# Optimization experiments

Measured on AMD Instinct MI355X. Metric: run time of the kernel, lower is better.

Reference implementation:

```python
import jax, jax.numpy as jnp
import numpy as np

DIM = 128; MOTION = 128; HEADS = 8; WS = 8; B2 = 4; H = 192; W = 192; HID = 512

def _ln(x, w, b, eps=1e-5):
    m = x.mean(-1, keepdims=True)
    v = ((x - m) ** 2).mean(-1, keepdims=True)
    return (x - m) / jnp.sqrt(v + eps) * w + b

def _win_part(x, ws):
    B, Hh, Ww, C = x.shape
    x = x.reshape(B, Hh // ws, ws, Ww // ws, ws, C).transpose(0, 1, 3, 2, 4, 5)
    return x.reshape(-1, ws * ws, C)

def _win_rev(win, ws, Hh, Ww):
    nwB, N, C = win.shape
    B = nwB // ((Hh // ws) * (Ww // ws))
    x = win.reshape(B, Hh // ws, Ww // ws, ws, ws, C).transpose(0, 1, 3, 2, 4, 5)
    return x.reshape(B, Hh, Ww, C)

def setup_inputs() -> dict:
    key = jax.random.key(0)
    ks = jax.random.split(key, 12)
    def lin(k, o, i):
        return jax.random.normal(k, (o, i), jnp.float32) * 0.02
    return {
        "x": jax.random.normal(ks[0], (B2, H * W, DIM), jnp.float32),
        "cor": jax.random.uniform(ks[1], (B2, H * W, 2), dtype=jnp.float32),
        "q_w": lin(ks[2], DIM, DIM),
        "kv_w": lin(ks[3], 2 * DIM, DIM),
        "cor_w": lin(ks[4], MOTION, 2),
        "proj_w": lin(ks[5], DIM, DIM), "proj_b": jnp.zeros((DIM,), jnp.float32),
        "mproj_w": lin(ks[6], MOTION, MOTION), "mproj_b": jnp.zeros((MOTION,), jnp.float32),
        "norm1_w": jnp.ones((DIM,), jnp.float32), "norm1_b": jnp.zeros((DIM,), jnp.float32),
        "norm2_w": jnp.ones((DIM,), jnp.float32), "norm2_b": jnp.zeros((DIM,), jnp.float32),
        "fc1_w": lin(ks[7], HID, DIM), "fc1_b": jnp.zeros((HID,), jnp.float32),
        "dw_w": jax.random.normal(ks[8], (HID, 1, 3, 3), jnp.float32) * 0.1,
        "dw_b": jnp.zeros((HID,), jnp.float32),
        "fc2_w": lin(ks[9], DIM, HID), "fc2_b": jnp.zeros((DIM,), jnp.float32),
    }

def _attn(x1, x2, cor, q_w, kv_w, cor_w, proj_w, proj_b, mproj_w, mproj_b):
    # x1,x2: (nwB, N, C) windowed query / cross-frame key-value; cor: (nwB, N, 2)
    B, N, C = x1.shape
    hd = C // HEADS
    mh = MOTION // HEADS
    scale = hd ** -0.5
    q = (x1 @ q_w.T).reshape(B, N, HEADS, hd).transpose(0, 2, 1, 3)
    kv = (x2 @ kv_w.T).reshape(B, N, 2, HEADS, hd).transpose(2, 0, 3, 1, 4)
    k, v = kv[0], kv[1]
    ce = cor @ cor_w.T                                   # (B, N, MOTION)
    ceh = ce.reshape(B, N, HEADS, mh).transpose(0, 2, 1, 3)
    attn = jax.nn.softmax(jnp.einsum('bhnd,bhmd->bhnm', q, k) * scale, axis=-1)
    xo = jnp.einsum('bhnm,bhmd->bhnd', attn, v).transpose(0, 2, 1, 3).reshape(B, N, C)
    crev = jnp.einsum('bhnm,bhmd->bhnd', attn, ceh).transpose(0, 2, 1, 3).reshape(B, N, MOTION)
    motion = (crev - ce) @ mproj_w.T + mproj_b
    return xo @ proj_w.T + proj_b, motion

def _mlp(x, fc1_w, fc1_b, dw_w, dw_b, fc2_w, fc2_b):
    B, N, _ = x.shape
    h = x @ fc1_w.T + fc1_b                              # (B, N, HID)
    hm = h.transpose(0, 2, 1).reshape(B, HID, H, W)
    hm = jax.lax.conv_general_dilated(hm, dw_w, (1, 1), 'SAME',
                                      feature_group_count=HID,
                                      dimension_numbers=('NCHW', 'OIHW', 'NCHW'))
    hm = hm + dw_b[None, :, None, None]
    h = jax.nn.gelu(hm.reshape(B, HID, N).transpose(0, 2, 1), approximate=False)
    return h @ fc2_w.T + fc2_b

def reference(x, cor, q_w, kv_w, cor_w, proj_w, proj_b, mproj_w, mproj_b,
              norm1_w, norm1_b, norm2_w, norm2_b, fc1_w, fc1_b, dw_w, dw_b, fc2_w, fc2_b):
    shortcut = x
    xn = _ln(x, norm1_w, norm1_b).reshape(B2, H, W, DIM)
    cm = cor.reshape(B2, H, W, 2)
    xw = _win_part(xn, WS)                               # (nwB, 64, DIM)
    cw = _win_part(cm, WS)
    nwB = xw.shape[0]
    xr = jnp.concatenate([xw[nwB // 2:], xw[:nwB // 2]], axis=0)
    xa, xm = _attn(xw, xr, cw, q_w, kv_w, cor_w, proj_w, proj_b, mproj_w, mproj_b)
    xa = _win_rev(xa, WS, H, W).reshape(B2, H * W, DIM)
    xm = _win_rev(xm, WS, H, W).reshape(B2, H * W, MOTION)
    x = shortcut + xa
    x = x + _mlp(_ln(x, norm2_w, norm2_b), fc1_w, fc1_b, dw_w, dw_b, fc2_w, fc2_b)
    return x, xm
```

## Files before the change

kernel.cpp:

```cpp
#include <hip/hip_runtime.h>
#include <hip/hip_bf16.h>
#include <math.h>

#define NB 4
#define IMG 192
#define HW (IMG*IMG)
#define T_TOT (NB*HW)
#define HID 512
#define NWB 2304
#define WPB 576
#define NWS 24

typedef __bf16 bf16;
typedef __bf16 bf8 __attribute__((ext_vector_type(8)));
typedef __bf16 bf4 __attribute__((ext_vector_type(4)));
typedef float f32x4 __attribute__((ext_vector_type(4)));

#define MFMA(a,b,c) __builtin_amdgcn_mfma_f32_16x16x32_bf16(a,b,c,0,0,0)

#define BAR_LGKM asm volatile("s_waitcnt lgkmcnt(0)\ns_barrier" ::: "memory")
#define BAR_ALL  asm volatile("s_waitcnt vmcnt(0) lgkmcnt(0)\ns_barrier" ::: "memory")

__device__ __forceinline__ int swz128(int row, int col){ return row*128 + (col ^ ((row&7)<<3)); }

__device__ __forceinline__ bf8 zero_bf8(){
  bf8 z = { (bf16)0.f,(bf16)0.f,(bf16)0.f,(bf16)0.f,(bf16)0.f,(bf16)0.f,(bf16)0.f,(bf16)0.f };
  return z;
}
__device__ __forceinline__ f32x4 zero_f4(){ f32x4 z = {0.f,0.f,0.f,0.f}; return z; }

typedef const __attribute__((address_space(1))) unsigned int as1_u32;
typedef __attribute__((address_space(3))) unsigned int as3_u32;
__device__ __forceinline__ void gload16(const bf16* g, bf16* l){
  __builtin_amdgcn_global_load_lds((as1_u32*)g, (as3_u32*)l, 16, 0, 0);
}

__global__ __launch_bounds__(256) void k_prep(
    const float* __restrict__ q_w, const float* __restrict__ kv_w,
    const float* __restrict__ proj_w, const float* __restrict__ fc1w,
    const float* __restrict__ fc2w, const float* __restrict__ mproj_w,
    const float* __restrict__ cor_w,
    bf16* __restrict__ wq, bf16* __restrict__ wkv, bf16* __restrict__ wpj,
    bf16* __restrict__ wf1, bf16* __restrict__ wf2, bf16* __restrict__ a2w)
{
  int idx = blockIdx.x*256 + threadIdx.x;
  if (idx < 16384){ wq[idx] = (bf16)(q_w[idx]*0.25f); return; }
  idx -= 16384;
  if (idx < 32768){ wkv[idx] = (bf16)kv_w[idx]; return; }
  idx -= 32768;
  if (idx < 16384){ wpj[idx] = (bf16)proj_w[idx]; return; }
  idx -= 16384;
  if (idx < 65536){ wf1[idx] = (bf16)fc1w[idx]; return; }
  idx -= 65536;
  if (idx < 65536){ wf2[idx] = (bf16)fc2w[idx]; return; }
  idx -= 65536;
  if (idx >= 4096) return;
  int o = idx >> 5, k = idx & 31;
  float acc = 0.f;
  if (k < 16){
    int h = k >> 1, c = k & 1;
    #pragma unroll
    for (int i=0;i<16;i++)
      acc += mproj_w[o*128 + h*16 + i] * cor_w[(h*16+i)*2 + c];
  }
  a2w[o*32 + k] = (bf16)acc;
}

__global__ __launch_bounds__(256) void k_attn(
    const float* __restrict__ x_in, const float* __restrict__ cor,
    const float* __restrict__ n1w, const float* __restrict__ n1b,
    const bf16* __restrict__ wq, const bf16* __restrict__ wkv,
    const bf16* __restrict__ wpj, const bf16* __restrict__ a2w,
    const float* __restrict__ proj_b, const float* __restrict__ mproj_b,
    bf16* __restrict__ x1, float* __restrict__ out_m)
{
  __shared__ __align__(16) bf16 s_s [64*128];
  __shared__ __align__(16) bf16 s_k [64*128];
  __shared__ __align__(16) bf16 s_vT[128*64];
  __shared__ __align__(16) bf16 s_P [64*64];
  __shared__ __align__(16) bf16 s_cT[16*64];
  __shared__ __align__(16) bf16 s_D [64*32];

  int tid = threadIdx.x, wm = tid>>6, l = tid&63;
  int lr = l & 15, lg = l >> 4;
  int win = blockIdx.x;
  int b  = win / WPB, wi = win % WPB;
  int wy = wi / NWS,  wx = wi % NWS;
  int bp = (b + NB/2) % NB;

  float cwf = 0.f;
  if (tid < 128){
    int m = tid >> 1, c = tid & 1;
    cwf = cor[((size_t)b*HW + (size_t)(wy*8+(m>>3))*IMG + wx*8+(m&7))*2 + c];
  }

  *(unsigned long long*)&s_D[tid*8]   = 0ull;
  *(unsigned long long*)&s_D[tid*8+4] = 0ull;
  if (tid >= 192){
    int cc = tid - 192;
    #pragma unroll
    for (int r=3;r<16;r++) s_cT[r*64 + cc] = (bf16)0.f;
  }
  if (tid < 128){
    int c = tid & 1, m = tid >> 1;
    s_cT[c*64 + (m ^ (c<<3))] = (bf16)cwf;
  } else if (tid < 192){
    int m = tid - 128;
    s_cT[2*64 + (m ^ 16)] = (bf16)1.0f;
  }

  {
    float4 nw0 = *(const float4*)(n1w + lr*8), nw1 = *(const float4*)(n1w + lr*8 + 4);
    float4 nb0 = *(const float4*)(n1b + lr*8), nb1 = *(const float4*)(n1b + lr*8 + 4);
    #pragma unroll
    for (int p=0;p<4;p++){
      int n = wm*16 + p*4 + lg;
      const float* xp = x_in + ((size_t)bp*HW + (size_t)(wy*8+(n>>3))*IMG + wx*8+(n&7))*128 + lr*8;
      float4 a = *(const float4*)xp;
      float4 b4 = *(const float4*)(xp+4);
      float s  = a.x+a.y+a.z+a.w + b4.x+b4.y+b4.z+b4.w;
      float sq = a.x*a.x+a.y*a.y+a.z*a.z+a.w*a.w + b4.x*b4.x+b4.y*b4.y+b4.z*b4.z+b4.w*b4.w;
      #pragma unroll
      for (int m=1;m<16;m<<=1){ s += __shfl_xor(s,m,16); sq += __shfl_xor(sq,m,16); }
      float mean = s*(1.f/128.f), var = sq*(1.f/128.f) - mean*mean;
      float rstd = rsqrtf(var + 1e-5f);
      bf8 o;
      o[0] = (bf16)((a.x -mean)*rstd*nw0.x + nb0.x);
      o[1] = (bf16)((a.y -mean)*rstd*nw0.y + nb0.y);
      o[2] = (bf16)((a.z -mean)*rstd*nw0.z + nb0.z);
      o[3] = (bf16)((a.w -mean)*rstd*nw0.w + nb0.w);
      o[4] = (bf16)((b4.x-mean)*rstd*nw1.x + nb1.x);
      o[5] = (bf16)((b4.y-mean)*rstd*nw1.y + nb1.y);
      o[6] = (bf16)((b4.z-mean)*rstd*nw1.z + nb1.z);
      o[7] = (bf16)((b4.w-mean)*rstd*nw1.w + nb1.w);
      *(bf8*)&s_s[swz128(n, lr*8)] = o;
    }
  }

  {
    bf8 af[4];
    #pragma unroll
    for (int ks=0;ks<4;ks++) af[ks] = *(const bf8*)&s_s[swz128(wm*16+lr, ks*32 + lg*8)];
    #pragma unroll
    for (int nt=0;nt<8;nt++){
      f32x4 acc = zero_f4();
      #pragma unroll
      for (int ks=0;ks<4;ks++){
        bf8 bfr = *(const bf8*)(wkv + (nt*16+lr)*128 + ks*32 + lg*8);
        acc = MFMA(af[ks], bfr, acc);
      }
      #pragma unroll
      for (int j=0;j<4;j++){
        int row = wm*16 + lg*4 + j;
        s_k[swz128(row, nt*16+lr)] = (bf16)acc[j];
      }
    }
    #pragma unroll
    for (int nt=0;nt<8;nt++){
      f32x4 acc = zero_f4();
      #pragma unroll
      for (int ks=0;ks<4;ks++){
        bf8 bfr = *(const bf8*)(wkv + (128 + nt*16+lr)*128 + ks*32 + lg*8);
        acc = MFMA(af[ks], bfr, acc);
      }
      #pragma unroll
      for (int j=0;j<4;j++){
        int tok = wm*16 + lg*4 + j;
        int chc = nt*16 + lr;
        s_vT[chc*64 + (tok ^ ((chc&7)<<3))] = (bf16)acc[j];
      }
    }
  }

  {
    float4 nw0 = *(const float4*)(n1w + lr*8), nw1 = *(const float4*)(n1w + lr*8 + 4);
    float4 nb0 = *(const float4*)(n1b + lr*8), nb1 = *(const float4*)(n1b + lr*8 + 4);
    #pragma unroll
    for (int p=0;p<4;p++){
      int n = wm*16 + p*4 + lg;
      const float* xp = x_in + ((size_t)b*HW + (size_t)(wy*8+(n>>3))*IMG + wx*8+(n&7))*128 + lr*8;
      float4 a = *(const float4*)xp;
      float4 b4 = *(const float4*)(xp+4);
      float s  = a.x+a.y+a.z+a.w + b4.x+b4.y+b4.z+b4.w;
      float sq = a.x*a.x+a.y*a.y+a.z*a.z+a.w*a.w + b4.x*b4.x+b4.y*b4.y+b4.z*b4.z+b4.w*b4.w;
      #pragma unroll
      for (int m=1;m<16;m<<=1){ s += __shfl_xor(s,m,16); sq += __shfl_xor(sq,m,16); }
      float mean = s*(1.f/128.f), var = sq*(1.f/128.f) - mean*mean;
      float rstd = rsqrtf(var + 1e-5f);
      bf8 o;
      o[0] = (bf16)((a.x -mean)*rstd*nw0.x + nb0.x);
      o[1] = (bf16)((a.y -mean)*rstd*nw0.y + nb0.y);
      o[2] = (bf16)((a.z -mean)*rstd*nw0.z + nb0.z);
      o[3] = (bf16)((a.w -mean)*rstd*nw0.w + nb0.w);
      o[4] = (bf16)((b4.x-mean)*rstd*nw1.x + nb1.x);
      o[5] = (bf16)((b4.y-mean)*rstd*nw1.y + nb1.y);
      o[6] = (bf16)((b4.z-mean)*rstd*nw1.z + nb1.z);
      o[7] = (bf16)((b4.w-mean)*rstd*nw1.w + nb1.w);
      *(bf8*)&s_s[swz128(n, lr*8)] = o;
    }
  }

  {
    bf8 af[4];
    #pragma unroll
    for (int ks=0;ks<4;ks++) af[ks] = *(const bf8*)&s_s[swz128(wm*16+lr, ks*32 + lg*8)];
    #pragma unroll
    for (int nt=0;nt<8;nt++){
      f32x4 acc = zero_f4();
      #pragma unroll
      for (int ks=0;ks<4;ks++){
        bf8 bfr = *(const bf8*)(wq + (nt*16+lr)*128 + ks*32 + lg*8);
        acc = MFMA(af[ks], bfr, acc);
      }
      #pragma unroll
      for (int j=0;j<4;j++){
        int row = wm*16 + lg*4 + j;
        s_s[swz128(row, nt*16+lr)] = (bf16)acc[j];
      }
    }
  }

  BAR_LGKM;

  float mycw[4] = {0.f,0.f,0.f,0.f};
  if (lr < 2){
    #pragma unroll
    for (int j=0;j<4;j++){
      int row = wm*16 + lg*4 + j;
      mycw[j] = (float)s_cT[lr*64 + (row ^ (lr<<3))];
    }
  }

  f32x4 accS[4];
  {
    bf8 aS = zero_bf8();
    if (l < 32) aS = *(const bf8*)&s_s[swz128(wm*16+lr, lg*8)];
    #pragma unroll
    for (int nt=0;nt<4;nt++){
      bf8 bSv = zero_bf8();
      if (l < 32) bSv = *(const bf8*)&s_k[swz128(nt*16+lr, lg*8)];
      accS[nt] = MFMA(aS, bSv, zero_f4());
    }
  }
  #pragma unroll
  for (int h=0;h<8;h++){
    #pragma unroll
    for (int nt=0;nt<4;nt++){
      #pragma unroll
      for (int j=0;j<4;j++){
        int row = wm*16 + lg*4 + j;
        s_P[row*64 + ((nt*16+lr) ^ ((row&7)<<3))] = (bf16)__expf(accS[nt][j]);
      }
    }
    if (h < 7){
      bf8 aS = zero_bf8();
      if (l < 32) aS = *(const bf8*)&s_s[swz128(wm*16+lr, (h+1)*16 + lg*8)];
      #pragma unroll
      for (int nt=0;nt<4;nt++){
        bf8 bSv = zero_bf8();
        if (l < 32) bSv = *(const bf8*)&s_k[swz128(nt*16+lr, (h+1)*16 + lg*8)];
        accS[nt] = MFMA(aS, bSv, zero_f4());
      }
    }
    f32x4 accO = zero_f4(), accPC = zero_f4();
    #pragma unroll
    for (int ks=0;ks<2;ks++){
      int rowA = wm*16 + lr;
      bf8 aP = *(const bf8*)&s_P[rowA*64 + ((ks*32 + lg*8) ^ ((rowA&7)<<3))];
      int chc = h*16 + lr;
      bf8 bV = *(const bf8*)&s_vT[chc*64 + ((ks*32 + lg*8) ^ ((chc&7)<<3))];
      accO = MFMA(aP, bV, accO);
      bf8 bC = *(const bf8*)&s_cT[lr*64 + ((ks*32 + lg*8) ^ ((lr&7)<<3))];
      accPC = MFMA(aP, bC, accPC);
    }
    #pragma unroll
    for (int j=0;j<4;j++){
      int row = wm*16 + lg*4 + j;
      float rs = __shfl(accPC[j], (l & 48) + 2, 64);
      float inv = __builtin_amdgcn_rcpf(rs);
      s_s[swz128(row, h*16+lr)] = (bf16)(accO[j]*inv);
      if (lr < 2)
        s_D[row*32 + ((2*h+lr) ^ ((row&3)<<3))] = (bf16)(accPC[j]*inv - mycw[j]);
    }
  }

  {
    bf8 af[4];
    #pragma unroll
    for (int ks=0;ks<4;ks++) af[ks] = *(const bf8*)&s_s[swz128(wm*16+lr, ks*32 + lg*8)];
    #pragma unroll
    for (int nt=0;nt<8;nt++){
      f32x4 acc = zero_f4();
      #pragma unroll
      for (int ks=0;ks<4;ks++){
        bf8 bfr = *(const bf8*)(wpj + (nt*16+lr)*128 + ks*32 + lg*8);
        acc = MFMA(af[ks], bfr, acc);
      }
      int col = nt*16 + lr;
      float pb = proj_b[col];
      #pragma unroll
      for (int j=0;j<4;j++){
        int tok = wm*16 + lg*4 + j;
        int yy = wy*8 + (tok>>3), xx = wx*8 + (tok&7);
        size_t addr = ((size_t)b*HW + yy*IMG + xx)*128 + col;
        x1[addr] = (bf16)(acc[j] + pb + x_in[addr]);
      }
    }
  }
  {
    int rowA = wm*16 + lr;
    bf8 afD = *(const bf8*)&s_D[rowA*32 + ((lg*8) ^ ((rowA&3)<<3))];
    #pragma unroll
    for (int nt=0;nt<8;nt++){
      bf8 bfr = *(const bf8*)(a2w + (nt*16+lr)*32 + lg*8);
      f32x4 acc = MFMA(afD, bfr, zero_f4());
      int col = nt*16 + lr;
      float pb = mproj_b[col];
      #pragma unroll
      for (int j=0;j<4;j++){
        int tok = wm*16 + lg*4 + j;
        int yy = wy*8 + (tok>>3), xx = wx*8 + (tok&7);
        size_t addr = ((size_t)b*HW + yy*IMG + xx)*128 + col;
        out_m[addr] = acc[j] + pb;
      }
    }
  }
}

__global__ __launch_bounds__(256) void k_fc1(
    const bf16* __restrict__ x1, const float* __restrict__ n2w, const float* __restrict__ n2b,
    const bf16* __restrict__ wf1, const float* __restrict__ fc1b, bf16* __restrict__ h)
{
  __shared__ __align__(16) bf16 s_a[64*128];
  int tid = threadIdx.x, wm = tid>>6, l = tid&63;
  int lr = l & 15, lg = l >> 4;
  size_t t0 = (size_t)blockIdx.x * 64;

  float4 nw0 = *(const float4*)(n2w + lr*8), nw1 = *(const float4*)(n2w + lr*8 + 4);
  float4 nb0 = *(const float4*)(n2b + lr*8), nb1 = *(const float4*)(n2b + lr*8 + 4);

  #pragma unroll
  for (int rr=0; rr<4; rr++){
    int row = wm*16 + rr*4 + lg;
    bf8 v = *(const bf8*)(x1 + (t0+row)*128 + lr*8);
    float xv8[8];
    #pragma unroll
    for (int k=0;k<8;k++) xv8[k] = (float)v[k];
    float s=0.f, sq=0.f;
    #pragma unroll
    for (int k=0;k<8;k++){ s += xv8[k]; sq += xv8[k]*xv8[k]; }
    #pragma unroll
    for (int m=1;m<16;m<<=1){ s += __shfl_xor(s,m,16); sq += __shfl_xor(sq,m,16); }
    float mean = s*(1.f/128.f), var = sq*(1.f/128.f) - mean*mean;
    float rstd = rsqrtf(var + 1e-5f);
    bf8 o;
    o[0] = (bf16)((xv8[0]-mean)*rstd*nw0.x + nb0.x);
    o[1] = (bf16)((xv8[1]-mean)*rstd*nw0.y + nb0.y);
    o[2] = (bf16)((xv8[2]-mean)*rstd*nw0.z + nb0.z);
    o[3] = (bf16)((xv8[3]-mean)*rstd*nw0.w + nb0.w);
    o[4] = (bf16)((xv8[4]-mean)*rstd*nw1.x + nb1.x);
    o[5] = (bf16)((xv8[5]-mean)*rstd*nw1.y + nb1.y);
    o[6] = (bf16)((xv8[6]-mean)*rstd*nw1.z + nb1.z);
    o[7] = (bf16)((xv8[7]-mean)*rstd*nw1.w + nb1.w);
    *(bf8*)&s_a[swz128(row, lr*8)] = o;
  }
  __syncthreads();

  bf8 af[4];
  #pragma unroll
  for (int ks=0;ks<4;ks++) af[ks] = *(const bf8*)&s_a[swz128(wm*16+lr, ks*32 + lg*8)];
  for (int ntb=0; ntb<4; ntb++){
    f32x4 acc[8];
    #pragma unroll
    for (int q8=0;q8<8;q8++){
      acc[q8] = zero_f4();
      #pragma unroll
      for (int ks=0;ks<4;ks++){
        int ocol = ntb*128 + q8*16 + lr;
        bf8 bfr = *(const bf8*)(wf1 + (size_t)ocol*128 + ks*32 + lg*8);
        acc[q8] = MFMA(af[ks], bfr, acc[q8]);
      }
    }
    #pragma unroll
    for (int q8=0;q8<8;q8++){
      int col = ntb*128 + q8*16 + lr;
      float bb = fc1b[col];
      #pragma unroll
      for (int j=0;j<4;j++){
        int tl = wm*16 + lg*4 + j;
        h[(t0+tl)*512 + col] = (bf16)(acc[q8][j] + bb);
      }
    }
  }
}

__global__ __launch_bounds__(256) void k_mlp2(
    const bf16* __restrict__ h, const float* __restrict__ dww, const float* __restrict__ dwb,
    const bf16* __restrict__ wf2, const float* __restrict__ fc2b,
    const bf16* __restrict__ x1, float* __restrict__ outx)
{
  __shared__ __align__(16) bf16 s_hh[2][100*128];
  int tid = threadIdx.x, wm = tid>>6, l = tid&63;
  int lr = l & 15, lg = l >> 4;
  int tile = 575 - blockIdx.x, b = 3 - blockIdx.y;
  int ty = tile / 24, tx = tile % 24;
  int cq = (tid & 31) * 4;
  int tg2 = tid >> 5;

  f32x4 acc[8];
  #pragma unroll
  for (int q=0;q<8;q++) acc[q] = zero_f4();

  bool edge = (ty==0) | (ty==23) | (tx==0) | (tx==23);
  if (edge){
    #pragma unroll
    for (int it=0; it<7; it++){
      int idx = it*256 + tid;
      if (idx < 1600){
        int pos = idx>>4, c0 = (idx&15)*8;
        int hy = pos/10, hx = pos%10;
        int yy = ty*8 + hy - 1, xx = tx*8 + hx - 1;
        if (yy<0 || yy>=IMG || xx<0 || xx>=IMG){
          *(bf8*)&s_hh[0][pos*128 + c0] = zero_bf8();
          *(bf8*)&s_hh[1][pos*128 + c0] = zero_bf8();
        }
      }
    }
  }

  #define STAGE_DMA(KC, BUF)                                                  \
    _Pragma("unroll")                                                         \
    for (int it=0; it<7; it++){                                               \
      int idx = it*256 + tid;                                                 \
      if (idx < 1600){                                                        \
        int pos = idx>>4, c0 = (idx&15)*8;                                    \
        int hy = pos/10, hx = pos%10;                                         \
        int yy = ty*8 + hy - 1, xx = tx*8 + hx - 1;                           \
        bf16* lb = &s_hh[BUF][it*2048 + wm*512];       \
        if (yy>=0 && yy<IMG && xx>=0 && xx<IMG)                               \
          gload16(h + ((size_t)b*HW + yy*IMG + xx)*512 + (KC)*128 + c0, lb);  \
      }                                                                       \
    }

  STAGE_DMA(0, 0);
  BAR_ALL;

  int cur = 0;
  for (int kc=0;kc<4;kc++){
    if (kc < 3) STAGE_DMA(kc+1, cur^1);

    int chg0 = kc*128 + cq;
    float4 bias4 = *(const float4*)(dwb + chg0);
    float cr[8][4];
    #pragma unroll
    for (int i=0;i<8;i++){ cr[i][0]=bias4.x; cr[i][1]=bias4.y; cr[i][2]=bias4.z; cr[i][3]=bias4.w; }
    #pragma unroll
    for (int dy=0;dy<3;dy++){
      float rv[10][4];
      #pragma unroll
      for (int p=0;p<10;p++){
        bf4 pv = *(const bf4*)&s_hh[cur][((tg2+dy)*10 + p)*128 + cq];
        rv[p][0]=(float)pv[0]; rv[p][1]=(float)pv[1];
        rv[p][2]=(float)pv[2]; rv[p][3]=(float)pv[3];
      }
      #pragma unroll
      for (int dx=0;dx<3;dx++){
        int tq = dy*3+dx;
        float w0 = dww[(chg0+0)*9 + tq];
        float w1 = dww[(chg0+1)*9 + tq];
        float w2 = dww[(chg0+2)*9 + tq];
        float w3 = dww[(chg0+3)*9 + tq];
        #pragma unroll
        for (int i=0;i<8;i++){
          cr[i][0] += rv[i+dx][0]*w0;
          cr[i][1] += rv[i+dx][1]*w1;
          cr[i][2] += rv[i+dx][2]*w2;
          cr[i][3] += rv[i+dx][3]*w3;
        }
      }
    }
    bf4 gout[8];
    #pragma unroll
    for (int i=0;i<8;i++){
      #pragma unroll
      for (int c=0;c<4;c++){
        float hv = cr[i][c];
        float hv2 = hv*hv;
        float v = hv * fmaf(hv2, -0.0713548353f, -1.5957691216f);
        float g = hv * __builtin_amdgcn_rcpf(1.0f + __expf(v));
        gout[i][c] = (bf16)g;
      }
    }
    BAR_LGKM;
    #pragma unroll
    for (int i=0;i<8;i++){
      int pos = (tg2+1)*10 + (i+1);
      *(bf4*)&s_hh[cur][pos*128 + (cq ^ (i<<3))] = gout[i];
    }
    {
      bf8 af[4];
      #pragma unroll
      for (int ks=0;ks<4;ks++){
        int tok = wm*16 + lr;
        int pos = ((tok>>3)+1)*10 + (tok&7) + 1;
        af[ks] = *(const bf8*)&s_hh[cur][pos*128 + ((ks*32 + lg*8) ^ ((lr&7)<<3))];
      }
      #pragma unroll
      for (int q=0;q<8;q++){
        #pragma unroll
        for (int ks=0;ks<4;ks++){
          bf8 bfr = *(const bf8*)(wf2 + (size_t)(q*16+lr)*512 + kc*128 + ks*32 + lg*8);
          acc[q] = MFMA(af[ks], bfr, acc[q]);
        }
      }
    }
    BAR_ALL;
    cur ^= 1;
  }
  #pragma unroll
  for (int q=0;q<8;q++){
    int col = q*16 + lr;
    float bb = fc2b[col];
    #pragma unroll
    for (int j=0;j<4;j++){
      int tok = wm*16 + lg*4 + j;
      int yy = ty*8 + (tok>>3), xx = tx*8 + (tok&7);
      size_t addr = ((size_t)b*HW + yy*IMG + xx)*128 + col;
      outx[addr] = acc[q][j] + bb + (float)x1[addr];
    }
  }
  #undef STAGE_DMA
}

extern "C" void kernel_launch(void* const* d_in, const int* in_sizes, int n_in,
                              void* d_out, int out_size, void* d_ws, size_t ws_size,
                              hipStream_t stream)
{
  const float* x      = (const float*)d_in[0];
  const float* cor    = (const float*)d_in[1];
  const float* q_w    = (const float*)d_in[2];
  const float* kv_w   = (const float*)d_in[3];
  const float* cor_w  = (const float*)d_in[4];
  const float* proj_w = (const float*)d_in[5];
  const float* proj_b = (const float*)d_in[6];
  const float* mproj_w= (const float*)d_in[7];
  const float* mproj_b= (const float*)d_in[8];
  const float* n1w    = (const float*)d_in[9];
  const float* n1b    = (const float*)d_in[10];
  const float* n2w    = (const float*)d_in[11];
  const float* n2b    = (const float*)d_in[12];
  const float* fc1w   = (const float*)d_in[13];
  const float* fc1b   = (const float*)d_in[14];
  const float* dww    = (const float*)d_in[15];
  const float* dwb    = (const float*)d_in[16];
  const float* fc2w   = (const float*)d_in[17];
  const float* fc2b   = (const float*)d_in[18];
  float* out = (float*)d_out;

  char* ws = (char*)d_ws;
  bf16* wq   = (bf16*)(ws + 0);
  bf16* wkv  = (bf16*)(ws + 32768);
  bf16* wpj  = (bf16*)(ws + 98304);
  bf16* a2w  = (bf16*)(ws + 131072);
  bf16* wf1  = (bf16*)(ws + 139264);
  bf16* wf2  = (bf16*)(ws + 270336);
  bf16* x1   = (bf16*)(ws + 401408);
  bf16* hbuf = (bf16*)(ws + 401408 + 37748736);

  k_prep<<<784, 256, 0, stream>>>(q_w, kv_w, proj_w, fc1w, fc2w, mproj_w, cor_w,
                                  wq, wkv, wpj, wf1, wf2, a2w);

  k_attn<<<NWB,      256, 0, stream>>>(x, cor, n1w, n1b, wq, wkv, wpj, a2w,
                                       proj_b, mproj_b,
                                       x1, out + (size_t)T_TOT*128);
  k_fc1 <<<T_TOT/64, 256, 0, stream>>>(x1, n2w, n2b, wf1, fc1b, hbuf);
  k_mlp2<<<dim3(576,4), 256, 0, stream>>>(hbuf, dww, dwb, wf2, fc2b, x1, out);
}
```

Measured before the change: 508.3 us.

## Fuse LayerNorm2 and fc1 into attention kernel epilogue

Folds the second LayerNorm and the fc1 projection into the attention kernel. The post-projection residual tile is kept in shared memory, so x1 no longer has to be re-read from global memory in a separate kernel, and one launch goes away. The cost is a longer attention kernel with more register pressure and more weight loads per block, and the hidden buffer is now written with a scattered window-to-image address pattern. The added barrier before the projection guards reuse of the shared buffers.

```diff
diff --git a/kernel.cpp b/kernel.cpp
--- a/kernel.cpp
+++ b/kernel.cpp
@@ -72,7 +72,9 @@
     const bf16* __restrict__ wq, const bf16* __restrict__ wkv,
     const bf16* __restrict__ wpj, const bf16* __restrict__ a2w,
     const float* __restrict__ proj_b, const float* __restrict__ mproj_b,
-    bf16* __restrict__ x1, float* __restrict__ out_m)
+    const float* __restrict__ n2w, const float* __restrict__ n2b,
+    const bf16* __restrict__ wf1, const float* __restrict__ fc1b,
+    bf16* __restrict__ x1, bf16* __restrict__ hb, float* __restrict__ out_m)
 {
   __shared__ __align__(16) bf16 s_s [64*128];
   __shared__ __align__(16) bf16 s_k [64*128];
@@ -284,6 +286,8 @@
     }
   }
 
+  BAR_LGKM;
+
   {
     bf8 af[4];
     #pragma unroll
@@ -303,7 +307,63 @@
         int tok = wm*16 + lg*4 + j;
         int yy = wy*8 + (tok>>3), xx = wx*8 + (tok&7);
         size_t addr = ((size_t)b*HW + yy*IMG + xx)*128 + col;
-        x1[addr] = (bf16)(acc[j] + pb + x_in[addr]);
+        bf16 bv = (bf16)(acc[j] + pb + x_in[addr]);
+        x1[addr] = bv;
+        s_k[swz128(tok, col)] = bv;
+      }
+    }
+  }
+  {
+    float4 nw0 = *(const float4*)(n2w + lr*8), nw1 = *(const float4*)(n2w + lr*8 + 4);
+    float4 nb0 = *(const float4*)(n2b + lr*8), nb1 = *(const float4*)(n2b + lr*8 + 4);
+    #pragma unroll
+    for (int p=0;p<4;p++){
+      int row = wm*16 + p*4 + lg;
+      bf8 v = *(const bf8*)&s_k[swz128(row, lr*8)];
+      float xv8[8];
+      #pragma unroll
+      for (int k2=0;k2<8;k2++) xv8[k2] = (float)v[k2];
+      float s=0.f, sq=0.f;
+      #pragma unroll
+      for (int k2=0;k2<8;k2++){ s += xv8[k2]; sq += xv8[k2]*xv8[k2]; }
+      #pragma unroll
+      for (int m=1;m<16;m<<=1){ s += __shfl_xor(s,m,16); sq += __shfl_xor(sq,m,16); }
+      float mean = s*(1.f/128.f), var = sq*(1.f/128.f) - mean*mean;
+      float rstd = rsqrtf(var + 1e-5f);
+      bf8 o;
+      o[0] = (bf16)((xv8[0]-mean)*rstd*nw0.x + nb0.x);
+      o[1] = (bf16)((xv8[1]-mean)*rstd*nw0.y + nb0.y);
+      o[2] = (bf16)((xv8[2]-mean)*rstd*nw0.z + nb0.z);
+      o[3] = (bf16)((xv8[3]-mean)*rstd*nw0.w + nb0.w);
+      o[4] = (bf16)((xv8[4]-mean)*rstd*nw1.x + nb1.x);
+      o[5] = (bf16)((xv8[5]-mean)*rstd*nw1.y + nb1.y);
+      o[6] = (bf16)((xv8[6]-mean)*rstd*nw1.z + nb1.z);
+      o[7] = (bf16)((xv8[7]-mean)*rstd*nw1.w + nb1.w);
+      *(bf8*)&s_s[swz128(row, lr*8)] = o;
+    }
+  }
+  {
+    bf8 af[4];
+    #pragma unroll
+    for (int ks=0;ks<4;ks++) af[ks] = *(const bf8*)&s_s[swz128(wm*16+lr, ks*32 + lg*8)];
+    for (int ntb=0; ntb<4; ntb++){
+      #pragma unroll
+      for (int q8=0;q8<8;q8++){
+        f32x4 acc = zero_f4();
+        #pragma unroll
+        for (int ks=0;ks<4;ks++){
+          int ocol = ntb*128 + q8*16 + lr;
+          bf8 bfr = *(const bf8*)(wf1 + (size_t)ocol*128 + ks*32 + lg*8);
+          acc = MFMA(af[ks], bfr, acc);
+        }
+        int col = ntb*128 + q8*16 + lr;
+        float bb = fc1b[col];
+        #pragma unroll
+        for (int j=0;j<4;j++){
+          int tok = wm*16 + lg*4 + j;
+          int yy = wy*8 + (tok>>3), xx = wx*8 + (tok&7);
+          hb[((size_t)b*HW + yy*IMG + xx)*512 + col] = (bf16)(acc[j] + bb);
+        }
       }
     }
   }
@@ -322,73 +382,6 @@
         int yy = wy*8 + (tok>>3), xx = wx*8 + (tok&7);
         size_t addr = ((size_t)b*HW + yy*IMG + xx)*128 + col;
         out_m[addr] = acc[j] + pb;
-      }
-    }
-  }
-}
-
-__global__ __launch_bounds__(256) void k_fc1(
-    const bf16* __restrict__ x1, const float* __restrict__ n2w, const float* __restrict__ n2b,
-    const bf16* __restrict__ wf1, const float* __restrict__ fc1b, bf16* __restrict__ h)
-{
-  __shared__ __align__(16) bf16 s_a[64*128];
-  int tid = threadIdx.x, wm = tid>>6, l = tid&63;
-  int lr = l & 15, lg = l >> 4;
-  size_t t0 = (size_t)blockIdx.x * 64;
-
-  float4 nw0 = *(const float4*)(n2w + lr*8), nw1 = *(const float4*)(n2w + lr*8 + 4);
-  float4 nb0 = *(const float4*)(n2b + lr*8), nb1 = *(const float4*)(n2b + lr*8 + 4);
-
-  #pragma unroll
-  for (int rr=0; rr<4; rr++){
-    int row = wm*16 + rr*4 + lg;
-    bf8 v = *(const bf8*)(x1 + (t0+row)*128 + lr*8);
-    float xv8[8];
-    #pragma unroll
-    for (int k=0;k<8;k++) xv8[k] = (float)v[k];
-    float s=0.f, sq=0.f;
-    #pragma unroll
-    for (int k=0;k<8;k++){ s += xv8[k]; sq += xv8[k]*xv8[k]; }
-    #pragma unroll
-    for (int m=1;m<16;m<<=1){ s += __shfl_xor(s,m,16); sq += __shfl_xor(sq,m,16); }
-    float mean = s*(1.f/128.f), var = sq*(1.f/128.f) - mean*mean;
-    float rstd = rsqrtf(var + 1e-5f);
-    bf8 o;
-    o[0] = (bf16)((xv8[0]-mean)*rstd*nw0.x + nb0.x);
-    o[1] = (bf16)((xv8[1]-mean)*rstd*nw0.y + nb0.y);
-    o[2] = (bf16)((xv8[2]-mean)*rstd*nw0.z + nb0.z);
-    o[3] = (bf16)((xv8[3]-mean)*rstd*nw0.w + nb0.w);
-    o[4] = (bf16)((xv8[4]-mean)*rstd*nw1.x + nb1.x);
-    o[5] = (bf16)((xv8[5]-mean)*rstd*nw1.y + nb1.y);
-    o[6] = (bf16)((xv8[6]-mean)*rstd*nw1.z + nb1.z);
-    o[7] = (bf16)((xv8[7]-mean)*rstd*nw1.w + nb1.w);
-    *(bf8*)&s_a[swz128(row, lr*8)] = o;
-  }
-  __syncthreads();
-
-  bf8 af[4];
-  #pragma unroll
-  for (int ks=0;ks<4;ks++) af[ks] = *(const bf8*)&s_a[swz128(wm*16+lr, ks*32 + lg*8)];
-  for (int ntb=0; ntb<4; ntb++){
-    f32x4 acc[8];
-    #pragma unroll
-    for (int q8=0;q8<8;q8++){
-      acc[q8] = zero_f4();
-      #pragma unroll
-      for (int ks=0;ks<4;ks++){
-        int ocol = ntb*128 + q8*16 + lr;
-        bf8 bfr = *(const bf8*)(wf1 + (size_t)ocol*128 + ks*32 + lg*8);
-        acc[q8] = MFMA(af[ks], bfr, acc[q8]);
-      }
-    }
-    #pragma unroll
-    for (int q8=0;q8<8;q8++){
-      int col = ntb*128 + q8*16 + lr;
-      float bb = fc1b[col];
-      #pragma unroll
-      for (int j=0;j<4;j++){
-        int tl = wm*16 + lg*4 + j;
-        h[(t0+tl)*512 + col] = (bf16)(acc[q8][j] + bb);
       }
     }
   }
@@ -571,8 +564,7 @@
                                   wq, wkv, wpj, wf1, wf2, a2w);
 
   k_attn<<<NWB,      256, 0, stream>>>(x, cor, n1w, n1b, wq, wkv, wpj, a2w,
-                                       proj_b, mproj_b,
-                                       x1, out + (size_t)T_TOT*128);
-  k_fc1 <<<T_TOT/64, 256, 0, stream>>>(x1, n2w, n2b, wf1, fc1b, hbuf);
+                                       proj_b, mproj_b, n2w, n2b, wf1, fc1b,
+                                       x1, hbuf, out + (size_t)T_TOT*128);
   k_mlp2<<<dim3(576,4), 256, 0, stream>>>(hbuf, dww, dwb, wf2, fc2b, x1, out);
 }
```

Result: slower. 601.8 us (+18.4%).
